# Kernel optimization log

Hardware: AMD Instinct MI355X
Metric: run time of the kernel (lower is better)

The kernel has to match this reference:

```python
import jax, jax.numpy as jnp
import numpy as np

B, T, I, H, O = 64, 512, 512, 1024, 512
K, N, M = 8, 128, 64  # mem_banks, memory_dims


def setup_inputs() -> dict:
    key = jax.random.key(0)
    ks = jax.random.split(key, 12)
    s = 0.05
    return {
        "x": jax.random.normal(ks[0], (B, T, 1, I), jnp.float32),
        "mem": jax.random.normal(ks[1], (K, N, M), jnp.float32) * s,
        "Wk": jax.random.normal(ks[2], (M, H), jnp.float32) * s,
        "bk": jnp.zeros((M,), jnp.float32),
        "Wri": jax.random.normal(ks[3], (I, M), jnp.float32) * s,  # read_to_in: M*num_reads -> I
        "bri": jnp.zeros((I,), jnp.float32),
        "Wih": jax.random.normal(ks[4], (3 * H, I), jnp.float32) * s,
        "Whh": jax.random.normal(ks[5], (3 * H, H), jnp.float32) * s,
        "bih": jnp.zeros((3 * H,), jnp.float32),
        "bhh": jnp.zeros((3 * H,), jnp.float32),
        "Wout": jax.random.normal(ks[6], (O, H), jnp.float32) * s,
        "bout": jnp.zeros((O,), jnp.float32),
    }


def reference(x, mem, Wk, bk, Wri, bri, Wih, Whh, bih, bhh, Wout, bout):
    b = x.shape[0]
    xt = x.reshape(b, x.shape[1], -1).transpose(1, 0, 2)  # (T, B, I)
    h0 = jnp.zeros((b, Whh.shape[1]), x.dtype)
    mem_flat = mem.reshape(-1, mem.shape[-1])  # (K*N, M)

    def step(h, x_t):
        # EMM content-based read over memory banks
        kq = h @ Wk.T + bk                                  # (B, M)
        scores = jnp.einsum('bm,pm->bp', kq, mem_flat)      # (B, K*N)
        w = jax.nn.softmax(scores, axis=-1)
        read = jnp.einsum('bp,pm->bm', w, mem_flat)         # (B, M)
        # controller: relu(read_to_in(read)) added to input, then GRUCell
        r = jax.nn.relu(read @ Wri.T + bri)                 # (B, I)
        xin = x_t + r
        gi = xin @ Wih.T + bih
        gh = h @ Whh.T + bhh
        i_r, i_z, i_n = jnp.split(gi, 3, axis=-1)
        h_r, h_z, h_n = jnp.split(gh, 3, axis=-1)
        rg = jax.nn.sigmoid(i_r + h_r)
        zg = jax.nn.sigmoid(i_z + h_z)
        ng = jnp.tanh(i_n + rg * h_n)
        h_new = (1.0 - zg) * ng + zg * h
        out = jax.nn.sigmoid(h_new @ Wout.T + bout)         # (B, O)
        return h_new, out

    _, outs = jax.lax.scan(step, h0, xt)                    # (T, B, O)
    return outs.transpose(1, 0, 2)                          # (B, T, O)
```

## Files before the change

kernel.cpp:

```cpp
#include <hip/hip_runtime.h>
#include <hip/hip_bf16.h>
#include <hip/hip_fp16.h>


typedef _Float16 half_t;
typedef _Float16 half8 __attribute__((ext_vector_type(8)));
typedef float f32x4 __attribute__((ext_vector_type(4)));

#define NB 64
#define NT 512
#define NI 512
#define NH 1024
#define G3 3072
#define NP 1024
#define NM 64
#define HB (NB * NH)
#define MTP 1032

#define NGH 96
#define NGI 32
#define NEMM 64
#define GRID (NGH + NGI + NEMM)

__device__ __forceinline__ float sigm(float v) { return 1.f / (1.f + __expf(-v)); }

union SM {
    half_t ghw[32 * 1024];
    half_t giw[96 * 512];
    struct {
        half_t memT[NM * MTP];
        half_t w16[NP];
        float  kqs[NM];
        float  rd[NM];
        float  red[512];
        float  mred[8], sred[8];
    } e;
};

__device__ __forceinline__ void gbar(unsigned* bar) {
    __syncthreads();
    if (threadIdx.x == 0) {
        unsigned* cnt = bar;
        unsigned* gen = bar + 32;
        __builtin_amdgcn_fence(__ATOMIC_RELEASE, "agent");
        unsigned g = __hip_atomic_load(gen, __ATOMIC_RELAXED, __HIP_MEMORY_SCOPE_AGENT);
        unsigned a = __hip_atomic_fetch_add(cnt, 1u, __ATOMIC_RELAXED, __HIP_MEMORY_SCOPE_AGENT);
        if (a == GRID - 1u) {
            __hip_atomic_store(cnt, 0u, __ATOMIC_RELAXED, __HIP_MEMORY_SCOPE_AGENT);
            __hip_atomic_store(gen, g + 1u, __ATOMIC_RELEASE, __HIP_MEMORY_SCOPE_AGENT);
        } else {
            while (__hip_atomic_load(gen, __ATOMIC_RELAXED, __HIP_MEMORY_SCOPE_AGENT) == g) {
                __builtin_amdgcn_s_sleep(4);
            }
        }
        __builtin_amdgcn_fence(__ATOMIC_ACQUIRE, "agent");
    }
    __syncthreads();
}

__global__ __launch_bounds__(256) void prep_kernel(
    const float* __restrict__ Whh, const float* __restrict__ Wih,
    const float* __restrict__ Wout, const float* __restrict__ mem,
    const float* __restrict__ Wk, const float* __restrict__ Wri,
    half_t* __restrict__ Whh_fm, half_t* __restrict__ Wih_fm,
    half_t* __restrict__ Wout16, half_t* __restrict__ memT16p,
    half_t* __restrict__ Wk16, half_t* __restrict__ Wri16,
    half_t* __restrict__ hist0, float* __restrict__ h32,
    unsigned* __restrict__ bar)
{
    size_t stride = (size_t)gridDim.x * blockDim.x;
    size_t t0 = (size_t)blockIdx.x * blockDim.x + threadIdx.x;
    for (size_t i = t0; i < (size_t)3145728; i += stride) {
        unsigned w = (unsigned)i & 32767u;
        int g = (int)(i >> 15);
        int ct = w >> 14, r = w & 16383;
        int kk = r >> 9, u = r & 511;
        int e = u & 7, rr = (u >> 3) & 15, kg = u >> 7;
        int srow = g * 32 + ct * 16 + rr, scol = kk * 32 + kg * 8 + e;
        Whh_fm[i] = (half_t)Whh[(size_t)srow * NH + scol];
    }
    for (size_t i = t0; i < (size_t)1572864; i += stride) {
        int gb = (int)(i / 49152);
        int w = (int)(i % 49152);
        int gt = w / 16384, r = w & 16383;
        int ct = r >> 13, r2 = r & 8191;
        int kk = r2 >> 9, u = r2 & 511;
        int e = u & 7, rr = (u >> 3) & 15, kg = u >> 7;
        int srow = gt * NH + gb * 32 + ct * 16 + rr, scol = kk * 32 + kg * 8 + e;
        Wih_fm[i] = (half_t)Wih[(size_t)srow * NI + scol];
    }
    for (size_t i = t0; i < (size_t)NI * NH; i += stride) Wout16[i] = (half_t)Wout[i];
    for (size_t i = t0; i < (size_t)NP * NM; i += stride) {
        int p = (int)(i >> 6), m = (int)(i & 63);
        memT16p[(size_t)m * MTP + p] = (half_t)mem[i];
    }
    for (size_t i = t0; i < (size_t)NM * NH; i += stride) Wk16[i] = (half_t)Wk[i];
    for (size_t i = t0; i < (size_t)NI * NM; i += stride) Wri16[i] = (half_t)Wri[i];
    for (size_t i = t0; i < (size_t)HB; i += stride) hist0[i] = (half_t)0.f;
    for (size_t i = t0; i < (size_t)2 * HB; i += stride) h32[i] = 0.f;
    if (t0 < 64) bar[t0] = 0u;
}

__global__ __launch_bounds__(512) void ntm_persist(
    half_t* __restrict__ hist, float* __restrict__ h32,
    const half_t* __restrict__ Whh_fm, const float* __restrict__ bhh,
    float* __restrict__ gh32,
    const half_t* __restrict__ Wih_fm, const float* __restrict__ bih,
    const float* __restrict__ x,
    const half_t* __restrict__ memT16p,
    const half_t* __restrict__ Wk16, const float* __restrict__ bk,
    const half_t* __restrict__ Wri16, const float* __restrict__ bri,
    half_t* __restrict__ xin16,
    unsigned* __restrict__ bar)
{
    __shared__ SM sm;
    const int bid = blockIdx.x, tid = threadIdx.x;

    if (bid < NGH) {
        const uint4* s = (const uint4*)(Whh_fm + (size_t)bid * 32768);
        uint4* d = (uint4*)sm.ghw;
        for (int i = tid; i < 4096; i += 512) d[i] = s[i];
    } else if (bid < NGH + NGI) {
        const uint4* s = (const uint4*)(Wih_fm + (size_t)(bid - NGH) * 49152);
        uint4* d = (uint4*)sm.giw;
        for (int i = tid; i < 6144; i += 512) d[i] = s[i];
    } else {
        const uint4* s = (const uint4*)memT16p;
        uint4* d = (uint4*)sm.e.memT;
        for (int i = tid; i < 8256; i += 512) d[i] = s[i];
    }
    __syncthreads();

    const int wv = tid >> 6, lane = tid & 63;
    const int mt = wv & 3, ct = wv >> 2;
    const int row = lane & 15, kg = lane >> 4;

    for (int t = 0; t < NT; ++t) {
        float* hprev = h32 + (size_t)(t & 1) * HB;
        float* hnext = h32 + (size_t)((t + 1) & 1) * HB;

        if (bid < NGH) {
            const half_t* ap = hist + (size_t)t * HB + (size_t)(mt * 16 + row) * NH + kg * 8;
            const half_t* bl = sm.ghw + ct * 16384 + (kg * 16 + row) * 8;
            f32x4 acc = {0.f, 0.f, 0.f, 0.f};
#pragma unroll
            for (int kk = 0; kk < 32; ++kk)
                acc = __builtin_amdgcn_mfma_f32_16x16x32_f16(
                    *(const half8*)(ap + kk * 32), *(const half8*)(bl + kk * 512), acc, 0, 0, 0);
            int n = bid * 32 + ct * 16 + row;
            float bb = bhh[n];
#pragma unroll
            for (int r = 0; r < 4; ++r)
                gh32[(size_t)(mt * 16 + kg * 4 + r) * G3 + n] = acc[r] + bb;
        } else if (bid >= NGH + NGI) {
            const int b = bid - (NGH + NGI);
            float xv = x[((size_t)b * NT + t) * NI + tid];
            const int m = tid & 63, q = tid >> 6;
            {
                const half_t* hp = hist + (size_t)t * HB + (size_t)b * NH + q * 128;
                const half_t* wk = Wk16 + (size_t)m * NH + q * 128;
                float s = 0.f;
#pragma unroll
                for (int j = 0; j < 128; j += 8) {
                    half8 hv = *(const half8*)(hp + j);
                    half8 wvv = *(const half8*)(wk + j);
#pragma unroll
                    for (int e2 = 0; e2 < 8; ++e2) s += (float)hv[e2] * (float)wvv[e2];
                }
                sm.e.red[tid] = s;
            }
            __syncthreads();
            if (tid < 64) {
                float s = bk[tid];
#pragma unroll
                for (int q2 = 0; q2 < 8; ++q2) s += sm.e.red[q2 * 64 + tid];
                sm.e.kqs[tid] = s;
            }
            __syncthreads();
            float s0 = 0.f, s1 = 0.f;
            {
                const half_t* mp0 = sm.e.memT + tid * 2;
#pragma unroll 8
                for (int m2 = 0; m2 < 64; ++m2) {
                    float km = sm.e.kqs[m2];
                    const half_t* mp = mp0 + m2 * MTP;
                    s0 += km * (float)mp[0];
                    s1 += km * (float)mp[1];
                }
            }
            float lmax = fmaxf(s0, s1);
            for (int o = 32; o; o >>= 1) lmax = fmaxf(lmax, __shfl_xor(lmax, o));
            if ((tid & 63) == 0) sm.e.mred[tid >> 6] = lmax;
            __syncthreads();
            float gmax = sm.e.mred[0];
#pragma unroll
            for (int q2 = 1; q2 < 8; ++q2) gmax = fmaxf(gmax, sm.e.mred[q2]);
            float e0 = __expf(s0 - gmax), e1 = __expf(s1 - gmax);
            float ls = e0 + e1;
            for (int o = 32; o; o >>= 1) ls += __shfl_xor(ls, o);
            if ((tid & 63) == 0) sm.e.sred[tid >> 6] = ls;
            sm.e.w16[tid * 2] = (half_t)e0;
            sm.e.w16[tid * 2 + 1] = (half_t)e1;
            __syncthreads();
            float wsum = 0.f;
#pragma unroll
            for (int q2 = 0; q2 < 8; ++q2) wsum += sm.e.sred[q2];
            float winv = 1.f / wsum;
            {
                const half_t* mp = sm.e.memT + m * MTP + q * 128;
                const half_t* wp = sm.e.w16 + q * 128;
                float s = 0.f;
#pragma unroll
                for (int p0 = 0; p0 < 128; p0 += 8) {
                    half8 mv = *(const half8*)(mp + p0);
                    half8 wv2 = *(const half8*)(wp + p0);
#pragma unroll
                    for (int e2 = 0; e2 < 8; ++e2) s += (float)mv[e2] * (float)wv2[e2];
                }
                sm.e.red[tid] = s;
            }
            __syncthreads();
            if (tid < 64) {
                float s = 0.f;
#pragma unroll
                for (int q2 = 0; q2 < 8; ++q2) s += sm.e.red[q2 * 64 + tid];
                sm.e.rd[tid] = s * winv;
            }
            __syncthreads();
            {
                const half_t* wr = Wri16 + (size_t)tid * NM;
                float s = bri[tid];
#pragma unroll
                for (int m2 = 0; m2 < 64; m2 += 8) {
                    half8 wv2 = *(const half8*)(wr + m2);
#pragma unroll
                    for (int e2 = 0; e2 < 8; ++e2) s += sm.e.rd[m2 + e2] * (float)wv2[e2];
                }
                s = fmaxf(s, 0.f) + xv;
                xin16[(size_t)b * NI + tid] = (half_t)s;
            }
        }
        gbar(bar);

        if (bid >= NGH && bid < NGH + NGI) {
            const int gb = bid - NGH;
            const half_t* ap = xin16 + (size_t)(mt * 16 + row) * NI + kg * 8;
            const half_t* bR = sm.giw + ct * 8192 + (kg * 16 + row) * 8;
            const half_t* bZ = bR + 16384;
            const half_t* bN = bR + 32768;
            f32x4 aR = {0.f,0.f,0.f,0.f}, aZ = {0.f,0.f,0.f,0.f}, aN = {0.f,0.f,0.f,0.f};
#pragma unroll
            for (int kk = 0; kk < 16; ++kk) {
                half8 a = *(const half8*)(ap + kk * 32);
                aR = __builtin_amdgcn_mfma_f32_16x16x32_f16(a, *(const half8*)(bR + kk * 512), aR, 0, 0, 0);
                aZ = __builtin_amdgcn_mfma_f32_16x16x32_f16(a, *(const half8*)(bZ + kk * 512), aZ, 0, 0, 0);
                aN = __builtin_amdgcn_mfma_f32_16x16x32_f16(a, *(const half8*)(bN + kk * 512), aN, 0, 0, 0);
            }
            int n = gb * 32 + ct * 16 + row;
            float biR = bih[n], biZ = bih[NH + n], biN = bih[2 * NH + n];
#pragma unroll
            for (int r = 0; r < 4; ++r) {
                int b2 = mt * 16 + kg * 4 + r;
                float ghr = gh32[(size_t)b2 * G3 + n];
                float ghz = gh32[(size_t)b2 * G3 + NH + n];
                float ghn = gh32[(size_t)b2 * G3 + 2 * NH + n];
                float rg = sigm(aR[r] + biR + ghr);
                float zg = sigm(aZ[r] + biZ + ghz);
                float ng = tanhf(aN[r] + biN + rg * ghn);
                float hp = hprev[(size_t)b2 * NH + n];
                float hn = (1.f - zg) * ng + zg * hp;
                hnext[(size_t)b2 * NH + n] = hn;
                hist[(size_t)(t + 1) * HB + (size_t)b2 * NH + n] = (half_t)hn;
            }
        }
        gbar(bar);
    }
}

__global__ __launch_bounds__(256) void out_kernel(
    const half_t* __restrict__ hist,
    const half_t* __restrict__ Wout16,
    const float* __restrict__ bout,
    float* __restrict__ out)
{
    int tid = threadIdx.x;
    int widx = tid >> 6, lane = tid & 63;
    int m0 = blockIdx.x * 64 + widx * 16;
    int row = lane & 15, kg = lane >> 4;
    const half_t* ap = hist + HB + (size_t)(m0 + row) * NH + kg * 8;
    for (int ctl = 0; ctl < 32; ++ctl) {
        int n0 = ctl * 16;
        const half_t* bp = Wout16 + (size_t)(n0 + row) * NH + kg * 8;
        f32x4 acc = {0.f, 0.f, 0.f, 0.f};
#pragma unroll
        for (int kk = 0; kk < 32; ++kk) {
            acc = __builtin_amdgcn_mfma_f32_16x16x32_f16(
                *(const half8*)(ap + kk * 32), *(const half8*)(bp + kk * 32), acc, 0, 0, 0);
        }
        int n = n0 + row;
        float bo = bout[n];
#pragma unroll
        for (int r = 0; r < 4; ++r) {
            int m = m0 + kg * 4 + r;
            int b2 = m & 63, tt = m >> 6;
            out[((size_t)b2 * NT + tt) * NI + n] = sigm(acc[r] + bo);
        }
    }
}

extern "C" void kernel_launch(void* const* d_in, const int* in_sizes, int n_in,
                              void* d_out, int out_size, void* d_ws, size_t ws_size,
                              hipStream_t stream) {
    const float* x    = (const float*)d_in[0];
    const float* mem  = (const float*)d_in[1];
    const float* Wk   = (const float*)d_in[2];
    const float* bk   = (const float*)d_in[3];
    const float* Wri  = (const float*)d_in[4];
    const float* bri  = (const float*)d_in[5];
    const float* Wih  = (const float*)d_in[6];
    const float* Whh  = (const float*)d_in[7];
    const float* bih  = (const float*)d_in[8];
    const float* bhh  = (const float*)d_in[9];
    const float* Wout = (const float*)d_in[10];
    const float* bout = (const float*)d_in[11];
    float* out = (float*)d_out;

    size_t off = 0;
    char* wsb = (char*)d_ws;
    auto carve = [&](size_t bytes) -> char* {
        char* p = wsb + off;
        off += (bytes + 255) & ~(size_t)255;
        return p;
    };
    half_t* Whh_fm  = (half_t*)carve((size_t)G3 * NH * 2);
    half_t* Wih_fm  = (half_t*)carve((size_t)G3 * NI * 2);
    half_t* Wout16  = (half_t*)carve((size_t)NI * NH * 2);
    half_t* memT16p = (half_t*)carve((size_t)NM * MTP * 2);
    half_t* Wk16    = (half_t*)carve((size_t)NM * NH * 2);
    half_t* Wri16   = (half_t*)carve((size_t)NI * NM * 2);
    half_t* hist    = (half_t*)carve((size_t)(NT + 1) * HB * 2);
    float*  h32     = (float*)carve((size_t)2 * HB * 4);
    float*  gh32    = (float*)carve((size_t)NB * G3 * 4);
    half_t* xin16   = (half_t*)carve((size_t)NB * NI * 2);
    unsigned* bar   = (unsigned*)carve(256);
    (void)ws_size; (void)in_sizes; (void)n_in; (void)out_size;

    prep_kernel<<<dim3(2048), dim3(256), 0, stream>>>(
        Whh, Wih, Wout, mem, Wk, Wri,
        Whh_fm, Wih_fm, Wout16, memT16p, Wk16, Wri16, hist, h32, bar);

    ntm_persist<<<dim3(GRID), dim3(512), 0, stream>>>(
        hist, h32, Whh_fm, bhh, gh32, Wih_fm, bih, x,
        memT16p, Wk16, bk, Wri16, bri, xin16, bar);

    out_kernel<<<dim3(512), dim3(256), 0, stream>>>(hist, Wout16, bout, out);
}
```

Baseline: 13.48 ms.

## Use monotonic counter barrier without fences and atomic relaxed cross-block stores

Replaces the generation-reset grid barrier with a monotonic counter compared against a per-step target, and drops the release/acquire fences. Cross-block data (gh32, xin, hist) is now written and read with relaxed agent-scope atomics, so values bypass non-coherent caches instead of relying on fences. xin is expanded into a per-timestep ring so later steps never overwrite a buffer that is still being read. Each barrier does one less atomic and no cache flush, but memory ordering now depends on relaxed atomics, and writes are packed into 32-bit words through lane shuffles.

```diff
diff --git a/kernel.cpp b/kernel.cpp
--- a/kernel.cpp
+++ b/kernel.cpp
@@ -37,23 +37,19 @@
     } e;
 };
 
-__device__ __forceinline__ void gbar(unsigned* bar) {
+__device__ __forceinline__ void gbar(unsigned* bar, unsigned bidx) {
     __syncthreads();
     if (threadIdx.x == 0) {
         unsigned* cnt = bar;
         unsigned* gen = bar + 32;
-        __builtin_amdgcn_fence(__ATOMIC_RELEASE, "agent");
-        unsigned g = __hip_atomic_load(gen, __ATOMIC_RELAXED, __HIP_MEMORY_SCOPE_AGENT);
         unsigned a = __hip_atomic_fetch_add(cnt, 1u, __ATOMIC_RELAXED, __HIP_MEMORY_SCOPE_AGENT);
-        if (a == GRID - 1u) {
-            __hip_atomic_store(cnt, 0u, __ATOMIC_RELAXED, __HIP_MEMORY_SCOPE_AGENT);
-            __hip_atomic_store(gen, g + 1u, __ATOMIC_RELEASE, __HIP_MEMORY_SCOPE_AGENT);
+        if (a == bidx * GRID - 1u) {
+            __hip_atomic_store(gen, bidx, __ATOMIC_RELAXED, __HIP_MEMORY_SCOPE_AGENT);
         } else {
-            while (__hip_atomic_load(gen, __ATOMIC_RELAXED, __HIP_MEMORY_SCOPE_AGENT) == g) {
+            while (__hip_atomic_load(gen, __ATOMIC_RELAXED, __HIP_MEMORY_SCOPE_AGENT) < bidx) {
                 __builtin_amdgcn_s_sleep(4);
             }
         }
-        __builtin_amdgcn_fence(__ATOMIC_ACQUIRE, "agent");
     }
     __syncthreads();
 }
@@ -110,7 +106,7 @@
     const half_t* __restrict__ memT16p,
     const half_t* __restrict__ Wk16, const float* __restrict__ bk,
     const half_t* __restrict__ Wri16, const float* __restrict__ bri,
-    half_t* __restrict__ xin16,
+    half_t* __restrict__ xinR,
     unsigned* __restrict__ bar)
 {
     __shared__ SM sm;
@@ -134,10 +130,12 @@
     const int wv = tid >> 6, lane = tid & 63;
     const int mt = wv & 3, ct = wv >> 2;
     const int row = lane & 15, kg = lane >> 4;
+    unsigned bidx = 0;
 
     for (int t = 0; t < NT; ++t) {
         float* hprev = h32 + (size_t)(t & 1) * HB;
         float* hnext = h32 + (size_t)((t + 1) & 1) * HB;
+        half_t* xin = xinR + (size_t)t * (NB * NI);
 
         if (bid < NGH) {
             const half_t* ap = hist + (size_t)t * HB + (size_t)(mt * 16 + row) * NH + kg * 8;
@@ -151,7 +149,8 @@
             float bb = bhh[n];
 #pragma unroll
             for (int r = 0; r < 4; ++r)
-                gh32[(size_t)(mt * 16 + kg * 4 + r) * G3 + n] = acc[r] + bb;
+                __hip_atomic_store(&gh32[(size_t)(mt * 16 + kg * 4 + r) * G3 + n],
+                                   acc[r] + bb, __ATOMIC_RELAXED, __HIP_MEMORY_SCOPE_AGENT);
         } else if (bid >= NGH + NGI) {
             const int b = bid - (NGH + NGI);
             float xv = x[((size_t)b * NT + t) * NI + tid];
@@ -237,14 +236,20 @@
                     for (int e2 = 0; e2 < 8; ++e2) s += sm.e.rd[m2 + e2] * (float)wv2[e2];
                 }
                 s = fmaxf(s, 0.f) + xv;
-                xin16[(size_t)b * NI + tid] = (half_t)s;
-            }
-        }
-        gbar(bar);
+                unsigned short u = __builtin_bit_cast(unsigned short, (half_t)s);
+                unsigned short un = (unsigned short)__shfl_xor((int)u, 1);
+                if ((tid & 1) == 0) {
+                    unsigned pack = (unsigned)u | ((unsigned)un << 16);
+                    __hip_atomic_store((unsigned*)&xin[(size_t)b * NI + tid], pack,
+                                       __ATOMIC_RELAXED, __HIP_MEMORY_SCOPE_AGENT);
+                }
+            }
+        }
+        gbar(bar, ++bidx);
 
         if (bid >= NGH && bid < NGH + NGI) {
             const int gb = bid - NGH;
-            const half_t* ap = xin16 + (size_t)(mt * 16 + row) * NI + kg * 8;
+            const half_t* ap = xin + (size_t)(mt * 16 + row) * NI + kg * 8;
             const half_t* bR = sm.giw + ct * 8192 + (kg * 16 + row) * 8;
             const half_t* bZ = bR + 16384;
             const half_t* bN = bR + 32768;
@@ -261,19 +266,28 @@
 #pragma unroll
             for (int r = 0; r < 4; ++r) {
                 int b2 = mt * 16 + kg * 4 + r;
-                float ghr = gh32[(size_t)b2 * G3 + n];
-                float ghz = gh32[(size_t)b2 * G3 + NH + n];
-                float ghn = gh32[(size_t)b2 * G3 + 2 * NH + n];
+                float ghr = __hip_atomic_load(&gh32[(size_t)b2 * G3 + n],
+                                              __ATOMIC_RELAXED, __HIP_MEMORY_SCOPE_AGENT);
+                float ghz = __hip_atomic_load(&gh32[(size_t)b2 * G3 + NH + n],
+                                              __ATOMIC_RELAXED, __HIP_MEMORY_SCOPE_AGENT);
+                float ghn = __hip_atomic_load(&gh32[(size_t)b2 * G3 + 2 * NH + n],
+                                              __ATOMIC_RELAXED, __HIP_MEMORY_SCOPE_AGENT);
                 float rg = sigm(aR[r] + biR + ghr);
                 float zg = sigm(aZ[r] + biZ + ghz);
                 float ng = tanhf(aN[r] + biN + rg * ghn);
                 float hp = hprev[(size_t)b2 * NH + n];
                 float hn = (1.f - zg) * ng + zg * hp;
                 hnext[(size_t)b2 * NH + n] = hn;
-                hist[(size_t)(t + 1) * HB + (size_t)b2 * NH + n] = (half_t)hn;
-            }
-        }
-        gbar(bar);
+                unsigned short u = __builtin_bit_cast(unsigned short, (half_t)hn);
+                unsigned short un = (unsigned short)__shfl_xor((int)u, 1);
+                if ((row & 1) == 0) {
+                    unsigned pack = (unsigned)u | ((unsigned)un << 16);
+                    __hip_atomic_store((unsigned*)&hist[(size_t)(t + 1) * HB + (size_t)b2 * NH + n],
+                                       pack, __ATOMIC_RELAXED, __HIP_MEMORY_SCOPE_AGENT);
+                }
+            }
+        }
+        gbar(bar, ++bidx);
     }
 }
 
@@ -341,8 +355,8 @@
     half_t* hist    = (half_t*)carve((size_t)(NT + 1) * HB * 2);
     float*  h32     = (float*)carve((size_t)2 * HB * 4);
     float*  gh32    = (float*)carve((size_t)NB * G3 * 4);
-    half_t* xin16   = (half_t*)carve((size_t)NB * NI * 2);
     unsigned* bar   = (unsigned*)carve(256);
+    half_t* xinR    = (half_t*)carve((size_t)NT * NB * NI * 2);
     (void)ws_size; (void)in_sizes; (void)n_in; (void)out_size;
 
     prep_kernel<<<dim3(2048), dim3(256), 0, stream>>>(
@@ -351,7 +365,7 @@
 
     ntm_persist<<<dim3(GRID), dim3(512), 0, stream>>>(
         hist, h32, Whh_fm, bhh, gh32, Wih_fm, bih, x,
-        memT16p, Wk16, bk, Wri16, bri, xin16, bar);
+        memT16p, Wk16, bk, Wri16, bri, xinR, bar);
 
     out_kernel<<<dim3(512), dim3(256), 0, stream>>>(hist, Wout16, bout, out);
 }
```

Result: faster. 11.03 ms (-18.2%).
